# Kernel optimization log

Hardware: AMD Instinct MI355X
Metric: run time of the kernel (lower is better)

## Reference

```python
import jax, jax.numpy as jnp
import numpy as np

R = 16       # voxel resolution
CH = 64      # channels
NSAMPLE = 16
PROJ = 3


def _bn(x, p, eps):
    # p: [4, C] rows = (gamma, beta, running_mean, running_var); eval-mode BN
    g, b, m, v = p
    sh = [1] * x.ndim
    sh[1] = -1
    return (x - m.reshape(sh)) * (g.reshape(sh) * jax.lax.rsqrt(v.reshape(sh) + eps)) + b.reshape(sh)


def _gather_ch(x, flat_idx):
    # x: [B, C, M], flat_idx: [B, L] -> [B, C, L]
    B, C, _ = x.shape
    idx = jnp.broadcast_to(flat_idx[:, None, :], (B, C, flat_idx.shape[1]))
    return jnp.take_along_axis(x, idx, axis=2)


def _pvb_forward(x, xyz, idx, w3d1, b3d1, bn3d1, w3d2, b3d2, bn3d2, proj_w1, proj_bn, proj_w2, pt_bn):
    B, C, N = x.shape
    r = R
    # ---------- voxelization (coords detached, normalize=False) ----------
    nc = xyz - xyz.mean(axis=2, keepdims=True)
    nc = jnp.clip((nc + 1.0) * 0.5 * r, 0.0, r - 1.0)
    nc = jax.lax.stop_gradient(nc)                        # [B,3,N] float in [0, r-1]
    vi = jnp.round(nc).astype(jnp.int32)
    flat = (vi[:, 0] * r + vi[:, 1]) * r + vi[:, 2]       # [B,N]
    seg = (flat + jnp.arange(B, dtype=jnp.int32)[:, None] * (r ** 3)).reshape(-1)
    feats = x.transpose(0, 2, 1).reshape(B * N, C)
    sums = jax.ops.segment_sum(feats, seg, num_segments=B * r ** 3)
    cnts = jax.ops.segment_sum(jnp.ones((B * N,), x.dtype), seg, num_segments=B * r ** 3)
    v = (sums / jnp.maximum(cnts, 1.0)[:, None]).reshape(B, r, r, r, C).transpose(0, 4, 1, 2, 3)
    # ---------- depthwise Conv3d -> BN3d -> LeakyReLU (x2) ----------
    dn = ('NCDHW', 'OIDHW', 'NCDHW')
    v = jax.lax.conv_general_dilated(v, w3d1, (1, 1, 1), 'SAME', dimension_numbers=dn,
                                     feature_group_count=C) + b3d1.reshape(1, C, 1, 1, 1)
    v = jax.nn.leaky_relu(_bn(v, bn3d1, 1e-4), 0.1)
    v = jax.lax.conv_general_dilated(v, w3d2, (1, 1, 1), 'SAME', dimension_numbers=dn,
                                     feature_group_count=C) + b3d2.reshape(1, C, 1, 1, 1)
    v = jax.nn.leaky_relu(_bn(v, bn3d2, 1e-4), 0.1)
    # ---------- trilinear devoxelize ----------
    vf = v.reshape(B, C, r ** 3)
    lo = jnp.floor(nc).astype(jnp.int32)
    fr = nc - lo
    hi = jnp.minimum(lo + 1, r - 1)
    p_v_x = jnp.zeros((B, C, N), x.dtype)
    for dx in (0, 1):
        for dy in (0, 1):
            for dz in (0, 1):
                xi = hi[:, 0] if dx else lo[:, 0]
                yi = hi[:, 1] if dy else lo[:, 1]
                zi = hi[:, 2] if dz else lo[:, 2]
                w = ((fr[:, 0] if dx else 1.0 - fr[:, 0]) *
                     (fr[:, 1] if dy else 1.0 - fr[:, 1]) *
                     (fr[:, 2] if dz else 1.0 - fr[:, 2]))
                p_v_x = p_v_x + w[:, None, :] * _gather_ch(vf, (xi * r + yi) * r + zi)
    # ---------- neighbor gather (precomputed ball-query idx) ----------
    K = idx.shape[-1]
    flat_nb = idx.reshape(B, N * K)
    x_j = _gather_ch(x, flat_nb).reshape(B, C, N, K)
    xyz_j = _gather_ch(xyz, flat_nb).reshape(B, 3, N, K)
    dp1 = xyz_j - xyz[:, :, :, None]                      # [B,3,N,K]
    df = x_j - x[:, :, :, None]                           # [B,C,N,K]
    # proj_conv: 1x1 conv -> BN2d -> ReLU -> 1x1 conv
    h = jnp.einsum('oc,bcnk->bonk', proj_w1, df)
    h = jax.nn.relu(_bn(h, proj_bn, 1e-5))
    dp2 = jnp.einsum('oc,bcnk->bonk', proj_w2, h)         # [B,3,N,K]
    dp = jnp.concatenate([dp1, dp2], axis=1)              # [B,6,N,K]
    # repeat_interleave of the 6 channels up to C (last gets remainder)
    part = 6
    rep = C // part
    repeats = np.array([rep] * (part - 1) + [C - rep * (part - 1)])
    w = jnp.repeat(dp, repeats, axis=1, total_repeat_length=C)
    x_j = x_j * w
    x_j = jax.nn.relu(_bn(x_j, pt_bn, 1e-5))              # proj_transform
    p_p_x = x_j.max(axis=-1)                              # max-pool over neighbors
    return p_v_x + p_p_x                                  # agg_way == 'add'


def setup_inputs() -> dict:
    key = jax.random.key(0)
    ks = jax.random.split(key, 16)
    B, C, N, K = 4, CH, 16384, NSAMPLE

    def bn_params(k, c):
        k1, k2, k3, k4 = jax.random.split(k, 4)
        return jnp.stack([1.0 + 0.1 * jax.random.normal(k1, (c,), jnp.float32),
                          0.1 * jax.random.normal(k2, (c,), jnp.float32),
                          0.1 * jax.random.normal(k3, (c,), jnp.float32),
                          jax.random.uniform(k4, (c,), jnp.float32, 0.5, 1.5)])

    return dict(
        x=jax.random.normal(ks[0], (B, C, N), jnp.float32),
        xyz=jax.random.uniform(ks[1], (B, 3, N), jnp.float32, -1.0, 1.0),
        idx=jax.random.randint(ks[2], (B, N, K), 0, N, jnp.int32),
        w3d1=0.1 * jax.random.normal(ks[3], (C, 1, 3, 3, 3), jnp.float32),
        b3d1=0.01 * jax.random.normal(ks[4], (C,), jnp.float32),
        bn3d1=bn_params(ks[5], C),
        w3d2=0.1 * jax.random.normal(ks[6], (C, 1, 3, 3, 3), jnp.float32),
        b3d2=0.01 * jax.random.normal(ks[7], (C,), jnp.float32),
        bn3d2=bn_params(ks[8], C),
        proj_w1=0.1 * jax.random.normal(ks[9], (PROJ, C), jnp.float32),
        proj_bn=bn_params(ks[10], PROJ),
        proj_w2=0.3 * jax.random.normal(ks[11], (PROJ, PROJ), jnp.float32),
        pt_bn=bn_params(ks[12], C),
    )


def reference(x, xyz, idx, w3d1, b3d1, bn3d1, w3d2, b3d2, bn3d2, proj_w1, proj_bn, proj_w2, pt_bn):
    return _pvb_forward(x, xyz, idx, w3d1, b3d1, bn3d1, w3d2, b3d2, bn3d2, proj_w1, proj_bn, proj_w2, pt_bn)
```

## Files before the change

kernel.cpp:

```cpp
#include <hip/hip_runtime.h>

namespace {
constexpr int B_  = 4;
constexpr int C_  = 64;
constexpr int N_  = 16384;
constexpr int K_  = 16;
constexpr int R3_ = 4096;

constexpr int OFF_MEANS = 0;
constexpr int OFF_XT    = 16;
constexpr int OFF_PTS   = OFF_XT   + B_*N_*C_/2;
constexpr int OFF_PTSH  = OFF_PTS  + B_*N_*8;
constexpr int OFF_DVT   = OFF_PTSH + B_*N_*4;
constexpr int OFF_SUMS  = OFF_DVT  + B_*N_*8;
constexpr int OFF_CNTS  = OFF_SUMS + B_*R3_*C_;
constexpr int OFF_VT16  = OFF_CNTS + B_*R3_;
constexpr int FILL_FLOATS = B_*R3_*C_ + B_*R3_;
constexpr int FILL_BLOCKS = FILL_FLOATS / (256 * 4);
}

__device__ __forceinline__ unsigned short f2bf(float f) {
  unsigned u = __float_as_uint(f);
  return (unsigned short)((u + 0x7FFFu + ((u >> 16) & 1u)) >> 16);
}
__device__ __forceinline__ float bf2f(unsigned short h) {
  return __uint_as_float(((unsigned)h) << 16);
}
__device__ __forceinline__ unsigned cvtpk_bf16(float lo, float hi) {
  unsigned r;
  asm("v_cvt_pk_bf16_f32 %0, %1, %2" : "=v"(r) : "v"(lo), "v"(hi));
  return r;
}
__device__ __forceinline__ float bflo(unsigned u) { return __uint_as_float(u << 16); }
__device__ __forceinline__ float bfhi(unsigned u) { return __uint_as_float(u & 0xffff0000u); }

__global__ __launch_bounds__(256) void k_init(
    const float* __restrict__ xyz, float* __restrict__ means,
    float* __restrict__ fill) {
  const int blk = blockIdx.x;
  if (blk >= 12) {
    const int base = (blk - 12) * (256 * 4) + threadIdx.x * 4;
    *(float4*)(fill + base) = make_float4(0.f, 0.f, 0.f, 0.f);
    return;
  }
  __shared__ double red[256];
  const float* p = xyz + blk * N_;
  double s = 0.0;
  for (int i = threadIdx.x; i < N_; i += 256) s += (double)p[i];
  red[threadIdx.x] = s;
  __syncthreads();
  for (int st = 128; st; st >>= 1) {
    if (threadIdx.x < st) red[threadIdx.x] += red[threadIdx.x + st];
    __syncthreads();
  }
  if (threadIdx.x == 0) means[blk] = (float)(red[0] * (1.0 / (double)N_));
}

__global__ __launch_bounds__(256) void k_prep(
    const float* __restrict__ x, const float* __restrict__ xyz,
    const float* __restrict__ pw1, const float* __restrict__ means,
    const float* __restrict__ ptbn,
    unsigned short* __restrict__ xT, float* __restrict__ pts,
    unsigned* __restrict__ ptsh, unsigned* __restrict__ dvt,
    float* __restrict__ sums, float* __restrict__ cnts) {
  __shared__ float tile[64 * 65];
  __shared__ float ncs[3][64];
  __shared__ float xys[3][64];
  __shared__ float hps[3][64];
  __shared__ float tss[64];
  __shared__ int   flats[64];

  const int t   = threadIdx.x;
  const int blk = blockIdx.x;
  const int b   = blk >> 8;
  const int n0  = (blk & 255) << 6;

  if (t < 64) tss[t] = ptbn[t] * rsqrtf(ptbn[192 + t] + 1e-5f);

#pragma unroll
  for (int i = 0; i < 4; ++i) {
    int c = i * 16 + (t >> 4);
    int j4 = (t & 15) * 4;
    float4 v = *(const float4*)&x[((size_t)(b * C_ + c)) * N_ + n0 + j4];
    tile[c * 65 + j4 + 0] = v.x;
    tile[c * 65 + j4 + 1] = v.y;
    tile[c * 65 + j4 + 2] = v.z;
    tile[c * 65 + j4 + 3] = v.w;
  }
  __syncthreads();

  unsigned* __restrict__ xT32 = (unsigned*)xT;
#pragma unroll
  for (int i = 0; i < 8; ++i) {
    int p = i * 8 + (t >> 5);
    int c2 = (t & 31) * 2;
    unsigned pk = cvtpk_bf16(tile[c2 * 65 + p] * tss[c2],
                             tile[(c2 + 1) * 65 + p] * tss[c2 + 1]);
    xT32[((size_t)(b * N_ + n0 + p)) * 32 + (t & 31)] = pk;
  }

  if (t < 192) {
    int p = t & 63, q = t >> 6;
    float s = 0.f;
#pragma unroll
    for (int c = 0; c < 64; ++c) s = fmaf(pw1[q * 64 + c], tile[c * 65 + p], s);
    size_t pb = ((size_t)(b * N_ + n0 + p)) * 8;
    pts[pb + 3 + q] = s;
    hps[q][p] = s;
    float v = xyz[((size_t)(b * 3 + q)) * N_ + n0 + p];
    pts[pb + q] = v;
    xys[q][p] = v;
    float nc = fminf(fmaxf((v - means[b * 3 + q] + 1.0f) * 8.0f, 0.0f), 15.0f);
    ncs[q][p] = nc;
  } else {
    int p = t & 63;
    size_t pb = ((size_t)(b * N_ + n0 + p)) * 8;
    pts[pb + 6] = 0.f;
    pts[pb + 7] = 0.f;
  }
  __syncthreads();

  if (t < 64) {
    const float nc0 = ncs[0][t], nc1 = ncs[1][t], nc2 = ncs[2][t];
    int vx = (int)rintf(nc0);
    int vy = (int)rintf(nc1);
    int vz = (int)rintf(nc2);
    int f = (vx * 16 + vy) * 16 + vz;
    flats[t] = f;
    atomicAdd(&cnts[b * R3_ + f], 1.0f);
    uint4 r;
    r.x = cvtpk_bf16(xys[0][t], xys[1][t]);
    r.y = cvtpk_bf16(xys[2][t], hps[0][t]);
    r.z = cvtpk_bf16(hps[1][t], hps[2][t]);
    r.w = 0u;
    *(uint4*)&ptsh[((size_t)(b * N_ + n0 + t)) * 4] = r;
    int lx = (int)nc0, ly = (int)nc1, lz = (int)nc2;
    float fx = nc0 - (float)lx, fy = nc1 - (float)ly, fz = nc2 - (float)lz;
    unsigned base = (unsigned)((lx * 16 + ly) * 16 + lz);
    unsigned w0 = base | (((unsigned)f2bf(fz)) << 16);
    unsigned w1 = cvtpk_bf16(fx, fy);
    *(uint2*)&dvt[((size_t)(b * N_ + n0 + t)) * 2] = make_uint2(w0, w1);
  }
  __syncthreads();

  const int w = t >> 6, lane = t & 63;
#pragma unroll
  for (int i = 0; i < 16; ++i) {
    int p = w * 16 + i;
    int f = flats[p];
    atomicAdd(&sums[((size_t)(b * R3_ + f)) * C_ + lane], tile[lane * 65 + p]);
  }
}

__global__ __launch_bounds__(256) void k_tr(
    const float* __restrict__ sums, const float* __restrict__ cnts,
    unsigned* __restrict__ vT16) {
  __shared__ float tile[64 * 65];
  __shared__ float rs[64];
  const int t = threadIdx.x;
  const int b = blockIdx.x >> 6;
  const int v0 = (blockIdx.x & 63) << 6;

#pragma unroll
  for (int i = 0; i < 16; ++i) {
    int r = i * 4 + (t >> 6);
    int c = t & 63;
    tile[r * 65 + c] = sums[((size_t)(b * R3_ + v0 + r)) * C_ + c];
  }
  if (t < 64) rs[t] = 1.0f / fmaxf(cnts[b * R3_ + v0 + t], 1.0f);
  __syncthreads();

#pragma unroll
  for (int i = 0; i < 8; ++i) {
    int d = t + i * 256;
    int c = d >> 5, vp = (d & 31) * 2;
    unsigned pk = cvtpk_bf16(tile[vp * 65 + c] * rs[vp],
                             tile[(vp + 1) * 65 + c] * rs[vp + 1]);
    vT16[((size_t)(b * C_ + c)) * 2048 + (v0 >> 1) + (d & 31)] = pk;
  }
}

__global__ __launch_bounds__(256, 8) void k_point(
    const unsigned short* __restrict__ xT, const float* __restrict__ pts,
    const unsigned* __restrict__ ptsh, const int* __restrict__ idx,
    const float* __restrict__ pbn, const float* __restrict__ pw2,
    const float* __restrict__ ptbn, float* __restrict__ out) {
  __shared__ unsigned w6[3][513];
  __shared__ int      jarr[512];
  __shared__ float    outT[64 * 33];

  const int t = threadIdx.x;
  const int blk = blockIdx.x;
  const int xcd = blk & 7;
  const int b = xcd >> 1;
  const int t32 = ((blk >> 3) << 1) | (xcd & 1);
  const int n0 = t32 * 32;

  const float psc0 = pbn[0] * rsqrtf(pbn[9]  + 1e-5f);
  const float psc1 = pbn[1] * rsqrtf(pbn[10] + 1e-5f);
  const float psc2 = pbn[2] * rsqrtf(pbn[11] + 1e-5f);
  const float pof0 = pbn[3] - pbn[6] * psc0;
  const float pof1 = pbn[4] - pbn[7] * psc1;
  const float pof2 = pbn[5] - pbn[8] * psc2;
  float W2r[9];
#pragma unroll
  for (int i = 0; i < 9; ++i) W2r[i] = pw2[i];

  const float* __restrict__ ptsb = pts + (size_t)b * N_ * 8;
  const unsigned* __restrict__ ptshb = ptsh + (size_t)b * N_ * 4;

#pragma unroll
  for (int rep = 0; rep < 2; ++rep) {
    const int q = t + rep * 256;
    const int p = q >> 4;
    const int n = n0 + p;
    const int j = idx[(size_t)b * N_ * K_ + (size_t)n0 * K_ + q];
    jarr[q] = j;
    uint4 q4 = *(const uint4*)(ptshb + (size_t)j * 4);
    const float qx0 = bflo(q4.x), qx1 = bfhi(q4.x);
    const float qx2 = bflo(q4.y), qh0 = bfhi(q4.y);
    const float qh1 = bflo(q4.z), qh2 = bfhi(q4.z);
    const float* ir = ptsb + (size_t)n * 8;
    float4 pa = *(const float4*)ir;
    float4 pb = *(const float4*)(ir + 4);
    float d0 = qx0 - pa.x, d1 = qx1 - pa.y, d2 = qx2 - pa.z;
    float c0 = pof0 - psc0 * pa.w;
    float c1 = pof1 - psc1 * pb.x;
    float c2 = pof2 - psc2 * pb.y;
    float h0 = fmaxf(fmaf(qh0, psc0, c0), 0.f);
    float h1 = fmaxf(fmaf(qh1, psc1, c1), 0.f);
    float h2 = fmaxf(fmaf(qh2, psc2, c2), 0.f);
    float e0 = fmaf(W2r[0], h0, fmaf(W2r[1], h1, W2r[2] * h2));
    float e1 = fmaf(W2r[3], h0, fmaf(W2r[4], h1, W2r[5] * h2));
    float e2 = fmaf(W2r[6], h0, fmaf(W2r[7], h1, W2r[8] * h2));
    w6[0][q] = cvtpk_bf16(d0, d1);
    w6[1][q] = cvtpk_bf16(d2, e0);
    w6[2][q] = cvtpk_bf16(e1, e2);
  }
  __syncthreads();

  const int w = t >> 6, lane = t & 63;
  const int half = lane >> 5;
  const int d = lane & 31;
  const int widx = d < 10 ? 0 : d < 20 ? 1 : 2;
  const bool hi = (d >= 5 && d < 10) || (d >= 15 && d < 20) || (d >= 25);
  const unsigned shl = hi ? 0u : 16u;
  const int c0i = 2 * d, c1i = 2 * d + 1;
  const float ts0 = ptbn[c0i] * rsqrtf(ptbn[192 + c0i] + 1e-5f);
  const float ts1 = ptbn[c1i] * rsqrtf(ptbn[192 + c1i] + 1e-5f);
  const float td0 = ptbn[64 + c0i] - ptbn[128 + c0i] * ts0;
  const float td1 = ptbn[64 + c1i] - ptbn[128 + c1i] * ts1;
  const unsigned* __restrict__ xT32b =
      (const unsigned*)xT + (size_t)b * N_ * 32;

#pragma unroll
  for (int i = 0; i < 4; ++i) {
    const int p = i * 8 + w + half * 4;
    const int pq = p * 16;

    unsigned xju[16], wfu[16];
#pragma unroll
    for (int k = 0; k < 16; ++k) {
      const int j = jarr[pq + k];
      xju[k] = xT32b[(size_t)j * 32 + d];
      wfu[k] = w6[widx][pq + k];
    }

    float pm0 = -3.0e38f, pm1 = -3.0e38f;
#pragma unroll
    for (int k = 0; k < 16; ++k) {
      float wf = __uint_as_float(wfu[k] << shl);
      float x0 = __uint_as_float(xju[k] << 16);
      float x1 = __uint_as_float(xju[k] & 0xffff0000u);
      pm0 = fmaxf(pm0, x0 * wf);
      pm1 = fmaxf(pm1, x1 * wf);
    }

    outT[c0i * 33 + p] = fmaxf(pm0 + td0, 0.f);
    outT[c1i * 33 + p] = fmaxf(pm1 + td1, 0.f);
  }
  __syncthreads();

#pragma unroll
  for (int i = 0; i < 8; ++i) {
    int c = i * 8 + (t >> 5);
    int col = t & 31;
    out[((size_t)(b * C_ + c)) * N_ + n0 + col] = outT[c * 33 + col];
  }
}

__global__ __launch_bounds__(512) void k_convdevox(
    const unsigned* __restrict__ vT16,
    const float* __restrict__ w3d1, const float* __restrict__ b3d1,
    const float* __restrict__ bn1, const float* __restrict__ w3d2,
    const float* __restrict__ b3d2, const float* __restrict__ bn2,
    const unsigned* __restrict__ dvt, float* __restrict__ out) {
  __shared__ float va[18 * 18 * 20];
  __shared__ float vb[18 * 18 * 20];
  __shared__ float vls[4370];
  const int t = threadIdx.x;
  const int b = blockIdx.x >> 6;
  const int c = blockIdx.x & 63;

  float W1[27], W2[27];
#pragma unroll
  for (int i = 0; i < 27; ++i) { W1[i] = w3d1[c * 27 + i]; W2[i] = w3d2[c * 27 + i]; }
  const float s1 = bn1[c] / sqrtf(bn1[192 + c] + 1e-4f);
  const float d1 = (b3d1[c] - bn1[128 + c]) * s1 + bn1[64 + c];
  const float s2 = bn2[c] / sqrtf(bn2[192 + c] + 1e-4f);
  const float d2 = (b3d2[c] - bn2[128 + c]) * s2 + bn2[64 + c];

  for (int i = t; i < 18 * 18 * 20; i += 512) { va[i] = 0.f; vb[i] = 0.f; }
  if (t < 274) vls[4096 + t] = 0.f;
  const unsigned* __restrict__ vrow = vT16 + ((size_t)(b * C_ + c)) * 2048;
  __syncthreads();

#pragma unroll
  for (int i = 0; i < 4; ++i) {
    int d = t + i * 512;
    unsigned u = vrow[d];
    int vox0 = d * 2;
    int z = vox0 & 15, yy = (vox0 >> 4) & 15, xx = vox0 >> 8;
    int base = ((xx + 1) * 18 + (yy + 1)) * 20 + (z + 1);
    va[base]     = bflo(u);
    va[base + 1] = bfhi(u);
  }
  __syncthreads();

  const int x = t >> 5, y = (t >> 1) & 15, z0 = (t & 1) * 8;
  float acc[8];

#pragma unroll
  for (int z = 0; z < 8; ++z) acc[z] = 0.f;
#pragma unroll
  for (int dx = 0; dx < 3; ++dx)
#pragma unroll
    for (int dy = 0; dy < 3; ++dy) {
      const float* row = &va[((x + dx) * 18 + (y + dy)) * 20 + z0];
      float wv[12];
      *(float4*)&wv[0] = *(const float4*)&row[0];
      *(float4*)&wv[4] = *(const float4*)&row[4];
      *(float4*)&wv[8] = *(const float4*)&row[8];
      const float k0 = W1[(dx * 3 + dy) * 3 + 0];
      const float k1 = W1[(dx * 3 + dy) * 3 + 1];
      const float k2 = W1[(dx * 3 + dy) * 3 + 2];
#pragma unroll
      for (int z = 0; z < 8; ++z)
        acc[z] = fmaf(k0, wv[z], fmaf(k1, wv[z + 1], fmaf(k2, wv[z + 2], acc[z])));
    }
  {
    const int wb = ((x + 1) * 18 + (y + 1)) * 20 + 1 + z0;
#pragma unroll
    for (int z = 0; z < 8; ++z) {
      float tt = acc[z] * s1 + d1;
      vb[wb + z] = tt > 0.f ? tt : 0.1f * tt;
    }
  }
  __syncthreads();

#pragma unroll
  for (int z = 0; z < 8; ++z) acc[z] = 0.f;
#pragma unroll
  for (int dx = 0; dx < 3; ++dx)
#pragma unroll
    for (int dy = 0; dy < 3; ++dy) {
      const float* row = &vb[((x + dx) * 18 + (y + dy)) * 20 + z0];
      float wv[12];
      *(float4*)&wv[0] = *(const float4*)&row[0];
      *(float4*)&wv[4] = *(const float4*)&row[4];
      *(float4*)&wv[8] = *(const float4*)&row[8];
      const float k0 = W2[(dx * 3 + dy) * 3 + 0];
      const float k1 = W2[(dx * 3 + dy) * 3 + 1];
      const float k2 = W2[(dx * 3 + dy) * 3 + 2];
#pragma unroll
      for (int z = 0; z < 8; ++z)
        acc[z] = fmaf(k0, wv[z], fmaf(k1, wv[z + 1], fmaf(k2, wv[z + 2], acc[z])));
    }
  {
    const int vbase = (x * 16 + y) * 16 + z0;
#pragma unroll
    for (int z = 0; z < 8; ++z) {
      float tt = acc[z] * s2 + d2;
      vls[vbase + z] = tt > 0.f ? tt : 0.1f * tt;
    }
  }
  __syncthreads();

  const uint2* __restrict__ dv2 = (const uint2*)(dvt + (size_t)b * N_ * 2);
  float* __restrict__ orow = out + ((size_t)(b * C_ + c)) * N_;
#pragma unroll 4
  for (int i = 0; i < 32; ++i) {
    const int n = t + i * 512;
    uint2 r = dv2[n];
    float o = orow[n];
    const int base = (int)(r.x & 0xffffu);
    const float fz = bfhi(r.x);
    const float fx = bflo(r.y), fy = bfhi(r.y);
    const float* v0 = &vls[base];
    float a0 = v0[0],   a1 = v0[1];
    float b0 = v0[16],  b1 = v0[17];
    float c0 = v0[256], c1 = v0[257];
    float d0 = v0[272], d1 = v0[273];
    float zA = fmaf(fz, a1 - a0, a0);
    float zB = fmaf(fz, b1 - b0, b0);
    float zC = fmaf(fz, c1 - c0, c0);
    float zD = fmaf(fz, d1 - d0, d0);
    float yAB = fmaf(fy, zB - zA, zA);
    float yCD = fmaf(fy, zD - zC, zC);
    orow[n] = o + fmaf(fx, yCD - yAB, yAB);
  }
}

extern "C" void kernel_launch(void* const* d_in, const int* in_sizes, int n_in,
                              void* d_out, int out_size, void* d_ws, size_t ws_size,
                              hipStream_t stream) {
  const float* x     = (const float*)d_in[0];
  const float* xyz   = (const float*)d_in[1];
  const int*   idx   = (const int*)  d_in[2];
  const float* w3d1  = (const float*)d_in[3];
  const float* b3d1  = (const float*)d_in[4];
  const float* bn3d1 = (const float*)d_in[5];
  const float* w3d2  = (const float*)d_in[6];
  const float* b3d2  = (const float*)d_in[7];
  const float* bn3d2 = (const float*)d_in[8];
  const float* pw1   = (const float*)d_in[9];
  const float* pbn   = (const float*)d_in[10];
  const float* pw2   = (const float*)d_in[11];
  const float* ptbn  = (const float*)d_in[12];
  float* out = (float*)d_out;
  float* ws  = (float*)d_ws;

  k_init<<<dim3(12 + FILL_BLOCKS), dim3(256), 0, stream>>>(
      xyz, ws + OFF_MEANS, ws + OFF_SUMS);
  k_prep<<<dim3(B_ * N_ / 64), dim3(256), 0, stream>>>(
      x, xyz, pw1, ws + OFF_MEANS, ptbn,
      (unsigned short*)(ws + OFF_XT), ws + OFF_PTS,
      (unsigned*)(ws + OFF_PTSH), (unsigned*)(ws + OFF_DVT),
      ws + OFF_SUMS, ws + OFF_CNTS);
  k_tr<<<dim3(B_ * 64), dim3(256), 0, stream>>>(
      ws + OFF_SUMS, ws + OFF_CNTS, (unsigned*)(ws + OFF_VT16));
  k_point<<<dim3(B_ * N_ / 32), dim3(256), 0, stream>>>(
      (const unsigned short*)(ws + OFF_XT), ws + OFF_PTS,
      (const unsigned*)(ws + OFF_PTSH), idx, pbn, pw2, ptbn, out);
  k_convdevox<<<dim3(B_ * C_), dim3(512), 0, stream>>>(
      (const unsigned*)(ws + OFF_VT16), w3d1, b3d1, bn3d1, w3d2, b3d2, bn3d2,
      (const unsigned*)(ws + OFF_DVT), out);
}
```

Measured before the change: 82.12 us.

## Merge transpose into point kernel and split conv from devoxelize

```diff
diff --git a/kernel.cpp b/kernel.cpp
--- a/kernel.cpp
+++ b/kernel.cpp
@@ -15,6 +15,7 @@
 constexpr int OFF_SUMS  = OFF_DVT  + B_*N_*8;
 constexpr int OFF_CNTS  = OFF_SUMS + B_*R3_*C_;
 constexpr int OFF_VT16  = OFF_CNTS + B_*R3_;
+constexpr int OFF_VOX2  = OFF_VT16 + B_*C_*R3_/2;
 constexpr int FILL_FLOATS = B_*R3_*C_ + B_*R3_;
 constexpr int FILL_BLOCKS = FILL_FLOATS / (256 * 4);
 }
@@ -22,9 +23,6 @@
 __device__ __forceinline__ unsigned short f2bf(float f) {
   unsigned u = __float_as_uint(f);
   return (unsigned short)((u + 0x7FFFu + ((u >> 16) & 1u)) >> 16);
-}
-__device__ __forceinline__ float bf2f(unsigned short h) {
-  return __uint_as_float(((unsigned)h) << 16);
 }
 __device__ __forceinline__ unsigned cvtpk_bf16(float lo, float hi) {
   unsigned r;
@@ -152,45 +150,45 @@
   }
 }
 
-__global__ __launch_bounds__(256) void k_tr(
-    const float* __restrict__ sums, const float* __restrict__ cnts,
-    unsigned* __restrict__ vT16) {
-  __shared__ float tile[64 * 65];
-  __shared__ float rs[64];
-  const int t = threadIdx.x;
-  const int b = blockIdx.x >> 6;
-  const int v0 = (blockIdx.x & 63) << 6;
-
-#pragma unroll
-  for (int i = 0; i < 16; ++i) {
-    int r = i * 4 + (t >> 6);
-    int c = t & 63;
-    tile[r * 65 + c] = sums[((size_t)(b * R3_ + v0 + r)) * C_ + c];
-  }
-  if (t < 64) rs[t] = 1.0f / fmaxf(cnts[b * R3_ + v0 + t], 1.0f);
-  __syncthreads();
-
-#pragma unroll
-  for (int i = 0; i < 8; ++i) {
-    int d = t + i * 256;
-    int c = d >> 5, vp = (d & 31) * 2;
-    unsigned pk = cvtpk_bf16(tile[vp * 65 + c] * rs[vp],
-                             tile[(vp + 1) * 65 + c] * rs[vp + 1]);
-    vT16[((size_t)(b * C_ + c)) * 2048 + (v0 >> 1) + (d & 31)] = pk;
-  }
-}
-
-__global__ __launch_bounds__(256, 8) void k_point(
+__global__ __launch_bounds__(256, 8) void k_pt_tr(
     const unsigned short* __restrict__ xT, const float* __restrict__ pts,
     const unsigned* __restrict__ ptsh, const int* __restrict__ idx,
     const float* __restrict__ pbn, const float* __restrict__ pw2,
-    const float* __restrict__ ptbn, float* __restrict__ out) {
-  __shared__ unsigned w6[3][513];
-  __shared__ int      jarr[512];
-  __shared__ float    outT[64 * 33];
-
+    const float* __restrict__ ptbn, float* __restrict__ out,
+    const float* __restrict__ sums, const float* __restrict__ cnts,
+    unsigned* __restrict__ vT16) {
+  __shared__ __align__(16) unsigned char smem[16896];
   const int t = threadIdx.x;
   const int blk = blockIdx.x;
+
+  if (blk >= 2048) {
+    float* tile = (float*)smem;
+    float* rs   = (float*)(smem + 16640);
+    const int bb = (blk - 2048) >> 6;
+    const int v0 = ((blk - 2048) & 63) << 6;
+#pragma unroll
+    for (int i = 0; i < 16; ++i) {
+      int r = i * 4 + (t >> 6);
+      int c = t & 63;
+      tile[r * 65 + c] = sums[((size_t)(bb * R3_ + v0 + r)) * C_ + c];
+    }
+    if (t < 64) rs[t] = 1.0f / fmaxf(cnts[bb * R3_ + v0 + t], 1.0f);
+    __syncthreads();
+#pragma unroll
+    for (int i = 0; i < 8; ++i) {
+      int d = t + i * 256;
+      int c = d >> 5, vp = (d & 31) * 2;
+      unsigned pk = cvtpk_bf16(tile[vp * 65 + c] * rs[vp],
+                               tile[(vp + 1) * 65 + c] * rs[vp + 1]);
+      vT16[((size_t)(bb * C_ + c)) * 2048 + (v0 >> 1) + (d & 31)] = pk;
+    }
+    return;
+  }
+
+  unsigned (*w6)[513] = (unsigned(*)[513])smem;
+  int*   jarr = (int*)(smem + 6156);
+  float* outT = (float*)(smem + 8204);
+
   const int xcd = blk & 7;
   const int b = xcd >> 1;
   const int t32 = ((blk >> 3) << 1) | (xcd & 1);
@@ -289,15 +287,14 @@
   }
 }
 
-__global__ __launch_bounds__(512) void k_convdevox(
+__global__ __launch_bounds__(256) void k_conv(
     const unsigned* __restrict__ vT16,
     const float* __restrict__ w3d1, const float* __restrict__ b3d1,
     const float* __restrict__ bn1, const float* __restrict__ w3d2,
     const float* __restrict__ b3d2, const float* __restrict__ bn2,
-    const unsigned* __restrict__ dvt, float* __restrict__ out) {
+    float* __restrict__ vox2) {
   __shared__ float va[18 * 18 * 20];
   __shared__ float vb[18 * 18 * 20];
-  __shared__ float vls[4370];
   const int t = threadIdx.x;
   const int b = blockIdx.x >> 6;
   const int c = blockIdx.x & 63;
@@ -310,16 +307,15 @@
   const float s2 = bn2[c] / sqrtf(bn2[192 + c] + 1e-4f);
   const float d2 = (b3d2[c] - bn2[128 + c]) * s2 + bn2[64 + c];
 
-  for (int i = t; i < 18 * 18 * 20; i += 512) { va[i] = 0.f; vb[i] = 0.f; }
-  if (t < 274) vls[4096 + t] = 0.f;
+  for (int i = t; i < 18 * 18 * 20; i += 256) { va[i] = 0.f; vb[i] = 0.f; }
   const unsigned* __restrict__ vrow = vT16 + ((size_t)(b * C_ + c)) * 2048;
   __syncthreads();
 
 #pragma unroll
-  for (int i = 0; i < 4; ++i) {
-    int d = t + i * 512;
-    unsigned u = vrow[d];
-    int vox0 = d * 2;
+  for (int i = 0; i < 8; ++i) {
+    int dd = t + i * 256;
+    unsigned u = vrow[dd];
+    int vox0 = dd * 2;
     int z = vox0 & 15, yy = (vox0 >> 4) & 15, xx = vox0 >> 8;
     int base = ((xx + 1) * 18 + (yy + 1)) * 20 + (z + 1);
     va[base]     = bflo(u);
@@ -327,31 +323,33 @@
   }
   __syncthreads();
 
-  const int x = t >> 5, y = (t >> 1) & 15, z0 = (t & 1) * 8;
-  float acc[8];
-
-#pragma unroll
-  for (int z = 0; z < 8; ++z) acc[z] = 0.f;
+  const int x = t >> 4, y = t & 15;
+  float acc[16];
+
+#pragma unroll
+  for (int z = 0; z < 16; ++z) acc[z] = 0.f;
 #pragma unroll
   for (int dx = 0; dx < 3; ++dx)
 #pragma unroll
     for (int dy = 0; dy < 3; ++dy) {
-      const float* row = &va[((x + dx) * 18 + (y + dy)) * 20 + z0];
-      float wv[12];
-      *(float4*)&wv[0] = *(const float4*)&row[0];
-      *(float4*)&wv[4] = *(const float4*)&row[4];
-      *(float4*)&wv[8] = *(const float4*)&row[8];
+      const float* row = &va[((x + dx) * 18 + (y + dy)) * 20];
+      float wv[18];
+      *(float4*)&wv[0]  = *(const float4*)&row[0];
+      *(float4*)&wv[4]  = *(const float4*)&row[4];
+      *(float4*)&wv[8]  = *(const float4*)&row[8];
+      *(float4*)&wv[12] = *(const float4*)&row[12];
+      wv[16] = row[16]; wv[17] = row[17];
       const float k0 = W1[(dx * 3 + dy) * 3 + 0];
       const float k1 = W1[(dx * 3 + dy) * 3 + 1];
       const float k2 = W1[(dx * 3 + dy) * 3 + 2];
 #pragma unroll
-      for (int z = 0; z < 8; ++z)
+      for (int z = 0; z < 16; ++z)
         acc[z] = fmaf(k0, wv[z], fmaf(k1, wv[z + 1], fmaf(k2, wv[z + 2], acc[z])));
     }
   {
-    const int wb = ((x + 1) * 18 + (y + 1)) * 20 + 1 + z0;
-#pragma unroll
-    for (int z = 0; z < 8; ++z) {
+    const int wb = ((x + 1) * 18 + (y + 1)) * 20 + 1;
+#pragma unroll
+    for (int z = 0; z < 16; ++z) {
       float tt = acc[z] * s1 + d1;
       vb[wb + z] = tt > 0.f ? tt : 0.1f * tt;
     }
@@ -359,38 +357,62 @@
   __syncthreads();
 
 #pragma unroll
-  for (int z = 0; z < 8; ++z) acc[z] = 0.f;
+  for (int z = 0; z < 16; ++z) acc[z] = 0.f;
 #pragma unroll
   for (int dx = 0; dx < 3; ++dx)
 #pragma unroll
     for (int dy = 0; dy < 3; ++dy) {
-      const float* row = &vb[((x + dx) * 18 + (y + dy)) * 20 + z0];
-      float wv[12];
-      *(float4*)&wv[0] = *(const float4*)&row[0];
-      *(float4*)&wv[4] = *(const float4*)&row[4];
-      *(float4*)&wv[8] = *(const float4*)&row[8];
+      const float* row = &vb[((x + dx) * 18 + (y + dy)) * 20];
+      float wv[18];
+      *(float4*)&wv[0]  = *(const float4*)&row[0];
+      *(float4*)&wv[4]  = *(const float4*)&row[4];
+      *(float4*)&wv[8]  = *(const float4*)&row[8];
+      *(float4*)&wv[12] = *(const float4*)&row[12];
+      wv[16] = row[16]; wv[17] = row[17];
       const float k0 = W2[(dx * 3 + dy) * 3 + 0];
       const float k1 = W2[(dx * 3 + dy) * 3 + 1];
       const float k2 = W2[(dx * 3 + dy) * 3 + 2];
 #pragma unroll
-      for (int z = 0; z < 8; ++z)
+      for (int z = 0; z < 16; ++z)
         acc[z] = fmaf(k0, wv[z], fmaf(k1, wv[z + 1], fmaf(k2, wv[z + 2], acc[z])));
     }
   {
-    const int vbase = (x * 16 + y) * 16 + z0;
-#pragma unroll
-    for (int z = 0; z < 8; ++z) {
+    const int vbase = (x * 16 + y) * 16;
+#pragma unroll
+    for (int z = 0; z < 16; ++z) {
       float tt = acc[z] * s2 + d2;
-      vls[vbase + z] = tt > 0.f ? tt : 0.1f * tt;
-    }
-  }
+      va[vbase + z] = tt > 0.f ? tt : 0.1f * tt;
+    }
+  }
+  __syncthreads();
+
+  float* __restrict__ orow = vox2 + ((size_t)(b * C_ + c)) * R3_;
+#pragma unroll
+  for (int i = 0; i < 16; ++i) orow[t + i * 256] = va[t + i * 256];
+}
+
+__global__ __launch_bounds__(256) void k_devox(
+    const float* __restrict__ vox2, const unsigned* __restrict__ dvt,
+    float* __restrict__ out) {
+  __shared__ float vls[4370];
+  const int t = threadIdx.x;
+  const int blk = blockIdx.x;
+  const int b = blk >> 8;
+  const int c = (blk >> 2) & 63;
+  const int q = blk & 3;
+
+  const float* __restrict__ vrow = vox2 + ((size_t)(b * C_ + c)) * R3_;
+#pragma unroll
+  for (int i = 0; i < 16; ++i) vls[t + i * 256] = vrow[t + i * 256];
+  if (t < 274) vls[4096 + t] = 0.f;
   __syncthreads();
 
   const uint2* __restrict__ dv2 = (const uint2*)(dvt + (size_t)b * N_ * 2);
   float* __restrict__ orow = out + ((size_t)(b * C_ + c)) * N_;
+  const int nb = q * 4096;
 #pragma unroll 4
-  for (int i = 0; i < 32; ++i) {
-    const int n = t + i * 512;
+  for (int i = 0; i < 16; ++i) {
+    const int n = nb + t + i * 256;
     uint2 r = dv2[n];
     float o = orow[n];
     const int base = (int)(r.x & 0xffffu);
@@ -437,12 +459,13 @@
       (unsigned short*)(ws + OFF_XT), ws + OFF_PTS,
       (unsigned*)(ws + OFF_PTSH), (unsigned*)(ws + OFF_DVT),
       ws + OFF_SUMS, ws + OFF_CNTS);
-  k_tr<<<dim3(B_ * 64), dim3(256), 0, stream>>>(
+  k_pt_tr<<<dim3(B_ * N_ / 32 + B_ * 64), dim3(256), 0, stream>>>(
+      (const unsigned short*)(ws + OFF_XT), ws + OFF_PTS,
+      (const unsigned*)(ws + OFF_PTSH), idx, pbn, pw2, ptbn, out,
       ws + OFF_SUMS, ws + OFF_CNTS, (unsigned*)(ws + OFF_VT16));
-  k_point<<<dim3(B_ * N_ / 32), dim3(256), 0, stream>>>(
-      (const unsigned short*)(ws + OFF_XT), ws + OFF_PTS,
-      (const unsigned*)(ws + OFF_PTSH), idx, pbn, pw2, ptbn, out);
-  k_convdevox<<<dim3(B_ * C_), dim3(512), 0, stream>>>(
+  k_conv<<<dim3(B_ * C_), dim3(256), 0, stream>>>(
       (const unsigned*)(ws + OFF_VT16), w3d1, b3d1, bn3d1, w3d2, b3d2, bn3d2,
-      (const unsigned*)(ws + OFF_DVT), out);
-}
+      ws + OFF_VOX2);
+  k_devox<<<dim3(B_ * C_ * 4), dim3(256), 0, stream>>>(
+      ws + OFF_VOX2, (const unsigned*)(ws + OFF_DVT), out);
+}
```

Measured after the change: 85.12 us. +3.6%, slower.
